# Kernel optimization log

Hardware: AMD Instinct MI355X
Metric: run time of the kernel (lower is better)

The kernel has to match this reference:

```python
import jax, jax.numpy as jnp
import numpy as np

N, D, L = 4096, 256, 3
E = 1.0  # eye scale 'e'


def _adj(X, W, b):
    # AdjLearner_intra: two Linear+ELU layers, then dense similarity h @ h.T -> [N, N]
    h = jax.nn.elu(X @ W[0] + b[0])
    h = jax.nn.elu(h @ W[1] + b[1])
    return h @ h.T


def _mlp(x, W, b, bn):
    # GIN MLP: Linear -> BatchNorm1d (batch stats, training mode) -> ReLU -> Linear
    h = x @ W[0] + b[0]
    mu = h.mean(axis=0)
    var = h.var(axis=0)  # biased, matches torch BN training normalization
    h = (h - mu) * jax.lax.rsqrt(var + 1e-5) * bn[0] + bn[1]
    return jax.nn.relu(h) @ W[1] + b[1]


def _gin(X, aW, ab, mW, mb, mbn):
    I = jnp.eye(X.shape[0], dtype=X.dtype)
    acc = jnp.zeros_like(X)
    for i in range(L):  # fixed small layer count
        adj = _adj(X, aW, ab)
        oh = (adj > adj.mean()).astype(X.dtype)  # adj_onehot: threshold at global mean
        X = _mlp((oh + E * I) @ X, mW[i], mb[i], mbn[i])
        acc = acc + X
    return acc / L


def setup_inputs() -> dict:
    key = jax.random.key(0)
    ks = jax.random.split(key, 16)
    s = np.float32(1.0 / np.sqrt(D))
    d = {}
    for i, name in enumerate(["QV", "Q", "V", "A"]):
        d[name] = jax.random.normal(ks[i], (N, D), jnp.float32)
    for j, br in enumerate(["qv", "t", "v"]):
        k0, k1 = ks[4 + 2 * j], ks[5 + 2 * j]
        d[f"adjW_{br}"] = jax.random.normal(k0, (2, D, D), jnp.float32) * s
        d[f"adjb_{br}"] = jnp.zeros((2, D), jnp.float32)
        d[f"mlpW_{br}"] = jax.random.normal(k1, (L, 2, D, D), jnp.float32) * s
        d[f"mlpb_{br}"] = jnp.zeros((L, 2, D), jnp.float32)
        d[f"mlpbn_{br}"] = jnp.stack(
            [jnp.ones((L, D), jnp.float32), jnp.zeros((L, D), jnp.float32)], axis=1
        )  # [L, 2(gamma,beta), D]
    return d


def reference(QV, Q, V, A,
              adjW_qv, adjb_qv, mlpW_qv, mlpb_qv, mlpbn_qv,
              adjW_t, adjb_t, mlpW_t, mlpb_t, mlpbn_t,
              adjW_v, adjb_v, mlpW_v, mlpb_v, mlpbn_v):
    GQV = _gin(QV, adjW_qv, adjb_qv, mlpW_qv, mlpb_qv, mlpbn_qv)  # type=1
    GQ = _gin(Q, adjW_t, adjb_t, mlpW_t, mlpb_t, mlpbn_t)          # type=2
    GV = _gin(V, adjW_v, adjb_v, mlpW_v, mlpb_v, mlpbn_v)          # type=3
    GA = _gin(A, adjW_t, adjb_t, mlpW_t, mlpb_t, mlpbn_t)          # type=2 (shared with Q branch)
    mse = lambda a, b: jnp.mean((a - b) ** 2)
    return (mse(GQV, GA), mse(GQ, GA), mse(GV, GA))
```

## Files before the change

### kernel.cpp

```cpp
#include <hip/hip_runtime.h>
#include <hip/hip_bf16.h>
#include <stdint.h>

#define NN 4096
#define DD 256
#define NL 3
typedef unsigned int uint;
typedef unsigned short ushort_t;

typedef float f32x4 __attribute__((ext_vector_type(4)));
typedef short bf16x8 __attribute__((ext_vector_type(8)));

struct Ptrs4 { const float* p0; const float* p1; const float* p2; const float* p3; };
__device__ __forceinline__ const float* sel(const Ptrs4& p, int b) {
    return b == 0 ? p.p0 : b == 1 ? p.p1 : b == 2 ? p.p2 : p.p3;
}

__device__ __forceinline__ uint pkbf2(float a, float b) {
    __hip_bfloat162 t = __float22bfloat162_rn(float2{a, b});
    union { __hip_bfloat162 h; uint u; } c; c.h = t; return c.u;
}
__device__ __forceinline__ void split3_pk(float a, float b, uint& h, uint& m, uint& l) {
    h = pkbf2(a, b);
    float ha = __uint_as_float(h << 16), hb = __uint_as_float(h & 0xFFFF0000u);
    float ra = a - ha, rb = b - hb;
    m = pkbf2(ra, rb);
    float ma = __uint_as_float(m << 16), mb = __uint_as_float(m & 0xFFFF0000u);
    l = pkbf2(ra - ma, rb - mb);
}

typedef __attribute__((address_space(3))) uint lds_u32;
typedef __attribute__((address_space(1))) const uint glb_u32;
__device__ __forceinline__ void gload16(void* l, const void* g) {
    __builtin_amdgcn_global_load_lds((glb_u32*)g, (lds_u32*)l, 16, 0, 0);
}
__device__ __forceinline__ void gload4(void* l, const void* g) {
    __builtin_amdgcn_global_load_lds((glb_u32*)g, (lds_u32*)l, 4, 0, 0);
}

template<int MODE>
__global__ __launch_bounds__(256, 4)
void gemm_small(const float* __restrict__ Xin, Ptrs4 Wp, Ptrs4 bp,
                float* __restrict__ Out, float* __restrict__ cs, float* __restrict__ csq,
                ushort_t* __restrict__ Hso)
{
    const int b = blockIdx.z;
    const float* Wb = sel(Wp, b);
    const float* bb = sel(bp, b);
    const float* X = Xin + (size_t)b * NN * DD;
    float* O = Out + (size_t)b * NN * DD;
    ushort_t* HsO = Hso + (size_t)b * 3 * (size_t)DD * NN;
    const int row0 = blockIdx.y * 128, col0 = blockIdx.x * 64;
    const int tid = threadIdx.x;
    __shared__ float Asm[16][132];
    __shared__ float Bsm[16][68];
    const int tr = (tid >> 4) << 3, tc = (tid & 15) << 2;
    const int m = tid & 127, kk = (tid >> 7) << 3;
    float acc[8][4] = {};
    for (int k0 = 0; k0 < DD; k0 += 16) {
        {
            const float* s1 = X + (size_t)(row0 + m) * DD + k0 + kk;
            float4 v0 = *(const float4*)s1, v1 = *(const float4*)(s1 + 4);
            Asm[kk+0][m]=v0.x; Asm[kk+1][m]=v0.y; Asm[kk+2][m]=v0.z; Asm[kk+3][m]=v0.w;
            Asm[kk+4][m]=v1.x; Asm[kk+5][m]=v1.y; Asm[kk+6][m]=v1.z; Asm[kk+7][m]=v1.w;
        }
        {
            const int k = tid >> 4, n = (tid & 15) << 2;
            *(float4*)&Bsm[k][n] = *(const float4*)(Wb + (size_t)(k0 + k) * DD + col0 + n);
        }
        __syncthreads();
        #pragma unroll
        for (int k = 0; k < 16; ++k) {
            float a[8], bv[4];
            *(float4*)&a[0] = *(const float4*)&Asm[k][tr];
            *(float4*)&a[4] = *(const float4*)&Asm[k][tr + 4];
            *(float4*)&bv[0] = *(const float4*)&Bsm[k][tc];
            #pragma unroll
            for (int i = 0; i < 8; ++i)
                #pragma unroll
                for (int j = 0; j < 4; ++j)
                    acc[i][j] = fmaf(a[i], bv[j], acc[i][j]);
        }
        __syncthreads();
    }
    float bias4[4];
    *(float4*)bias4 = *(const float4*)(bb + col0 + tc);
    float s4[4] = {0.f,0.f,0.f,0.f}, q4[4] = {0.f,0.f,0.f,0.f};
    const int dph = col0 + tc;
    const size_t sb3 = (size_t)(dph >> 3) * (NN * 8) + (dph & 4);
    #pragma unroll
    for (int i = 0; i < 8; ++i) {
        float ov[4];
        #pragma unroll
        for (int j = 0; j < 4; ++j) {
            float v = acc[i][j] + bias4[j];
            if (MODE == 0 || MODE == 1 || MODE == 3) v = (v > 0.f) ? v : (expf(v) - 1.f);
            ov[j] = v;
            if (MODE == 1 || MODE == 3) s4[j] += v;
            if (MODE == 2) { s4[j] += v; q4[j] += v * v; }
        }
        if (MODE == 3) {
            uint2 vh, vm, vl;
            split3_pk(ov[0], ov[1], vh.x, vm.x, vl.x);
            split3_pk(ov[2], ov[3], vh.y, vm.y, vl.y);
            size_t off = sb3 + (size_t)(row0 + tr + i) * 8;
            *(uint2*)(HsO + off) = vh;
            *(uint2*)(HsO + (size_t)DD * NN + off) = vm;
            *(uint2*)(HsO + (size_t)2 * DD * NN + off) = vl;
        } else {
            float4 o; o.x = ov[0]; o.y = ov[1]; o.z = ov[2]; o.w = ov[3];
            *(float4*)(O + (size_t)(row0 + tr + i) * DD + col0 + tc) = o;
        }
    }
    if (MODE == 1 || MODE == 2 || MODE == 3) {
        __syncthreads();
        const int rg = tid >> 4;
        #pragma unroll
        for (int j = 0; j < 4; ++j) {
            Asm[rg][tc + j] = s4[j];
            if (MODE == 2) Bsm[rg][tc + j] = q4[j];
        }
        __syncthreads();
        if (tid < 64) {
            float s = 0.f, q = 0.f;
            #pragma unroll
            for (int r = 0; r < 16; ++r) { s += Asm[r][tid]; if (MODE == 2) q += Bsm[r][tid]; }
            atomicAdd(&cs[b * DD + col0 + tid], s);
            if (MODE == 2) atomicAdd(&csq[b * DD + col0 + tid], q);
        }
    }
}

__global__ void thresh_k(const float* __restrict__ cs, float* __restrict__ tvals)
{
    const int b = blockIdx.x, t = threadIdx.x;
    __shared__ float red[256];
    float v = cs[b * DD + t];
    red[t] = v * v;
    __syncthreads();
    for (int s = 128; s > 0; s >>= 1) { if (t < s) red[t] += red[t + s]; __syncthreads(); }
    if (t == 0) tvals[b] = red[0] * (1.0f / 16777216.0f);
}

__global__ __launch_bounds__(256)
void tsplit_x(const float* __restrict__ Xin, ushort_t* __restrict__ Sh,
              ushort_t* __restrict__ Sm, ushort_t* __restrict__ Sl)
{
    const int b = blockIdx.z;
    const int n0 = blockIdx.x * 64, d0 = blockIdx.y * 64;
    const float* X = Xin + (size_t)b * NN * DD;
    __shared__ float ls[64][65];
    const int tid = threadIdx.x;
    #pragma unroll
    for (int i = 0; i < 4; ++i) {
        int u = (i << 8) + tid;
        int r = u >> 4, c4 = (u & 15) << 2;
        float4 v = *(const float4*)(X + (size_t)(n0 + r) * DD + d0 + c4);
        ls[r][c4] = v.x; ls[r][c4+1] = v.y; ls[r][c4+2] = v.z; ls[r][c4+3] = v.w;
    }
    __syncthreads();
    const int d = tid >> 2, seg = (tid & 3) << 4;
    uint ph[8], pm[8], pl[8];
    #pragma unroll
    for (int jj = 0; jj < 8; ++jj) {
        float a = ls[seg + 2 * jj][d];
        float c = ls[seg + 2 * jj + 1][d];
        split3_pk(a, c, ph[jj], pm[jj], pl[jj]);
    }
    size_t idx = ((size_t)(b * DD + d0 + d)) * NN + n0 + seg;
    *(uint4*)(Sh + idx)     = *(uint4*)&ph[0];
    *(uint4*)(Sh + idx + 8) = *(uint4*)&ph[4];
    *(uint4*)(Sm + idx)     = *(uint4*)&pm[0];
    *(uint4*)(Sm + idx + 8) = *(uint4*)&pm[4];
    *(uint4*)(Sl + idx)     = *(uint4*)&pl[0];
    *(uint4*)(Sl + idx + 8) = *(uint4*)&pl[4];
}

__global__ __launch_bounds__(256, 3)
void adj_mfma_s(const float* __restrict__ H, const float* __restrict__ tvals,
                uint8_t* __restrict__ mask)
{
    int t = blockIdx.x;
    int by = 0, rem = 32;
    while (t >= rem) { t -= rem; rem--; by++; }
    const int bx = by + t;
    const int b = blockIdx.z;
    const int row0 = by * 128, col0 = bx * 128;
    const int tid = threadIdx.x;
    const int wave = tid >> 6, ln = tid & 15, quad = (tid >> 4) & 3;
    const int wrow = wave >> 1, wcol = wave & 1;
    const float* Hb = H + (size_t)b * NN * DD;
    uint8_t* Mb = mask + (size_t)b * NN * (NN / 8);
    __shared__ ushort_t hs[2][3][128][34];

    f32x4 acc[4][4] = {};
    for (int k0 = 0; k0 < DD; k0 += 32) {
        #pragma unroll
        for (int i = 0; i < 8; ++i) {
            int f = (i << 8) + tid;
            int sr = f >> 3;
            int side = sr >> 7, r = sr & 127, part = f & 7;
            int grow = (side ? col0 : row0) + r;
            float4 v = *(const float4*)(Hb + (size_t)grow * DD + k0 + part * 4);
            uint h0, m0, l0, h1, m1, l1;
            split3_pk(v.x, v.y, h0, m0, l0);
            split3_pk(v.z, v.w, h1, m1, l1);
            uint2 ph; ph.x = h0; ph.y = h1;
            uint2 pm; pm.x = m0; pm.y = m1;
            uint2 pl; pl.x = l0; pl.y = l1;
            *(uint2*)&hs[side][0][r][part * 4] = ph;
            *(uint2*)&hs[side][1][r][part * 4] = pm;
            *(uint2*)&hs[side][2][r][part * 4] = pl;
        }
        __syncthreads();
        bf16x8 af[4][3];
        #pragma unroll
        for (int mt = 0; mt < 4; ++mt)
            #pragma unroll
            for (int lvl = 0; lvl < 3; ++lvl)
                af[mt][lvl] = *(const bf16x8*)&hs[0][lvl][wrow * 64 + mt * 16 + ln][quad * 8];
        #pragma unroll
        for (int nt = 0; nt < 4; ++nt) {
            int n = wcol * 64 + nt * 16 + ln;
            bf16x8 bh = *(const bf16x8*)&hs[1][0][n][quad * 8];
            bf16x8 bm = *(const bf16x8*)&hs[1][1][n][quad * 8];
            bf16x8 bl = *(const bf16x8*)&hs[1][2][n][quad * 8];
            #pragma unroll
            for (int mt = 0; mt < 4; ++mt) {
                f32x4 a = acc[mt][nt];
                a = __builtin_amdgcn_mfma_f32_16x16x32_bf16(af[mt][0], bh, a, 0, 0, 0);
                a = __builtin_amdgcn_mfma_f32_16x16x32_bf16(af[mt][0], bm, a, 0, 0, 0);
                a = __builtin_amdgcn_mfma_f32_16x16x32_bf16(af[mt][1], bh, a, 0, 0, 0);
                a = __builtin_amdgcn_mfma_f32_16x16x32_bf16(af[mt][0], bl, a, 0, 0, 0);
                a = __builtin_amdgcn_mfma_f32_16x16x32_bf16(af[mt][2], bh, a, 0, 0, 0);
                a = __builtin_amdgcn_mfma_f32_16x16x32_bf16(af[mt][1], bm, a, 0, 0, 0);
                acc[mt][nt] = a;
            }
        }
        __syncthreads();
    }
    const float t2 = tvals[b];
    #pragma unroll
    for (int mt = 0; mt < 4; ++mt)
        #pragma unroll
        for (int nt = 0; nt < 4; ++nt) {
            bool p0 = acc[mt][nt][0] > t2, p1 = acc[mt][nt][1] > t2;
            bool p2 = acc[mt][nt][2] > t2, p3 = acc[mt][nt][3] > t2;
            unsigned long long bal[4];
            bal[0] = __ballot(p0); bal[1] = __ballot(p1);
            bal[2] = __ballot(p2); bal[3] = __ballot(p3);
            if ((tid & 63) < 16) {
                int q = ln >> 2, rsel = ln & 3;
                unsigned long long bv = rsel == 0 ? bal[0] : rsel == 1 ? bal[1]
                                       : rsel == 2 ? bal[2] : bal[3];
                ushort_t u16 = (ushort_t)((bv >> (q * 16)) & 0xFFFFull);
                int row = row0 + wrow * 64 + mt * 16 + ln;
                int colb = (col0 + wcol * 64 + nt * 16) >> 3;
                *(ushort_t*)(Mb + (size_t)row * (NN / 8) + colb) = u16;
            }
            uint nib = (p0 ? 1u : 0u) | (p1 ? 2u : 0u) | (p2 ? 4u : 0u) | (p3 ? 8u : 0u);
            uint other = (uint)__shfl_xor((int)nib, 16);
            if ((quad & 1) == 0) {
                uint byt = nib | (other << 4);
                int rowm = col0 + wcol * 64 + nt * 16 + ln;
                int colbm = ((row0 + wrow * 64 + mt * 16) >> 3) + (quad >> 1);
                Mb[(size_t)rowm * (NN / 8) + colbm] = (uint8_t)byt;
            }
        }
}

__global__ __launch_bounds__(256, 3)
void adj_mfma_v2(const ushort_t* __restrict__ Hs, const float* __restrict__ tvals,
                 uint8_t* __restrict__ mask)
{
    int t = blockIdx.x;
    int by = 0, rem = 32;
    while (t >= rem) { t -= rem; rem--; by++; }
    const int bx = by + t;
    const int b = blockIdx.z;
    const int row0 = by * 128, col0 = bx * 128;
    const int tid = threadIdx.x;
    const int wave = tid >> 6, ln = tid & 15, quad = (tid >> 4) & 3;
    const int wrow = wave >> 1, wcol = wave & 1;
    const ushort_t* Hb = Hs + (size_t)b * 3 * (size_t)DD * NN;
    uint8_t* Mb = mask + (size_t)b * NN * (NN / 8);
    __shared__ ushort_t hs2[6][4][128][8];

    const int grow = tid & 127;
    const int qb = tid >> 7;
    const size_t var0 = (size_t)qb * (NN * 8) + (size_t)(row0 + grow) * 8;
    const size_t var1 = (size_t)qb * (NN * 8) + (size_t)(col0 + grow) * 8;

    f32x4 acc[4][4] = {};
    for (int kb0 = 0; kb0 < DD / 8; kb0 += 4) {
        #pragma unroll
        for (int c = 0; c < 12; ++c) {
            const int sl = c >> 1, part = c & 1;
            const int side = sl / 3, lvl = sl % 3;
            const ushort_t* g = Hb + (size_t)lvl * DD * NN
                                   + (size_t)(kb0 + part * 2) * (NN * 8)
                                   + (side ? var1 : var0);
            char* l = (char*)&hs2[0][0][0][0] + (((sl * 8 + part * 4 + wave)) << 10);
            gload16(l, g);
        }
        __syncthreads();
        bf16x8 af[4][3];
        #pragma unroll
        for (int mt = 0; mt < 4; ++mt)
            #pragma unroll
            for (int lvl = 0; lvl < 3; ++lvl)
                af[mt][lvl] = *(const bf16x8*)&hs2[lvl][quad][wrow * 64 + mt * 16 + ln][0];
        #pragma unroll
        for (int nt = 0; nt < 4; ++nt) {
            const int n = wcol * 64 + nt * 16 + ln;
            bf16x8 bh = *(const bf16x8*)&hs2[3][quad][n][0];
            bf16x8 bm = *(const bf16x8*)&hs2[4][quad][n][0];
            bf16x8 bl = *(const bf16x8*)&hs2[5][quad][n][0];
            #pragma unroll
            for (int mt = 0; mt < 4; ++mt) {
                f32x4 a = acc[mt][nt];
                a = __builtin_amdgcn_mfma_f32_16x16x32_bf16(af[mt][0], bh, a, 0, 0, 0);
                a = __builtin_amdgcn_mfma_f32_16x16x32_bf16(af[mt][0], bm, a, 0, 0, 0);
                a = __builtin_amdgcn_mfma_f32_16x16x32_bf16(af[mt][1], bh, a, 0, 0, 0);
                a = __builtin_amdgcn_mfma_f32_16x16x32_bf16(af[mt][0], bl, a, 0, 0, 0);
                a = __builtin_amdgcn_mfma_f32_16x16x32_bf16(af[mt][2], bh, a, 0, 0, 0);
                a = __builtin_amdgcn_mfma_f32_16x16x32_bf16(af[mt][1], bm, a, 0, 0, 0);
                acc[mt][nt] = a;
            }
        }
        __syncthreads();
    }
    const float t2 = tvals[b];
    #pragma unroll
    for (int mt = 0; mt < 4; ++mt)
        #pragma unroll
        for (int nt = 0; nt < 4; ++nt) {
            bool p0 = acc[mt][nt][0] > t2, p1 = acc[mt][nt][1] > t2;
            bool p2 = acc[mt][nt][2] > t2, p3 = acc[mt][nt][3] > t2;
            unsigned long long bal[4];
            bal[0] = __ballot(p0); bal[1] = __ballot(p1);
            bal[2] = __ballot(p2); bal[3] = __ballot(p3);
            if ((tid & 63) < 16) {
                int q = ln >> 2, rsel = ln & 3;
                unsigned long long bv = rsel == 0 ? bal[0] : rsel == 1 ? bal[1]
                                       : rsel == 2 ? bal[2] : bal[3];
                ushort_t u16 = (ushort_t)((bv >> (q * 16)) & 0xFFFFull);
                int row = row0 + wrow * 64 + mt * 16 + ln;
                int colb = (col0 + wcol * 64 + nt * 16) >> 3;
                *(ushort_t*)(Mb + (size_t)row * (NN / 8) + colb) = u16;
            }
            uint nib = (p0 ? 1u : 0u) | (p1 ? 2u : 0u) | (p2 ? 4u : 0u) | (p3 ? 8u : 0u);
            uint other = (uint)__shfl_xor((int)nib, 16);
            if ((quad & 1) == 0) {
                uint byt = nib | (other << 4);
                int rowm = col0 + wcol * 64 + nt * 16 + ln;
                int colbm = ((row0 + wrow * 64 + mt * 16) >> 3) + (quad >> 1);
                Mb[(size_t)rowm * (NN / 8) + colbm] = (uint8_t)byt;
            }
        }
}

__global__ __launch_bounds__(256)
void masked_mfma(float* __restrict__ Xio, const ushort_t* __restrict__ Sh,
                 const ushort_t* __restrict__ Sm, const ushort_t* __restrict__ Sl,
                 const uint8_t* __restrict__ mask)
{
    const int b = blockIdx.z;
    const int row0 = blockIdx.y * 128, col0 = blockIdx.x * 64;
    const int tid = threadIdx.x;
    const int wave = tid >> 6, ln = tid & 15, quad = (tid >> 4) & 3;
    const int wrow = wave >> 1, wcol = wave & 1;
    float* X = Xio + (size_t)b * NN * DD;
    const size_t sb = (size_t)b * DD * NN;
    const ushort_t* Ss[3] = { Sh + sb, Sm + sb, Sl + sb };
    const uint* Mw = (const uint*)(mask + (size_t)b * NN * (NN / 8));
    __shared__ ushort_t bt2[2][3][2][64][32];
    __shared__ uint msk2[2][2][128];

    const int c = tid >> 2;
    const int qp = (tid & 3) ^ ((tid >> 3) & 3);
    const size_t goff = (size_t)(col0 + c) * NN + (size_t)qp * 8;
    const size_t mrow = (size_t)(row0 + (tid & 127)) * 128;

    f32x4 acc[4][2] = {};

    #define STAGE(buf, t)                                                         \
        {                                                                         \
            const size_t j_ = (size_t)(t) * 64;                                   \
            _Pragma("unroll")                                                     \
            for (int lvl = 0; lvl < 3; ++lvl) {                                   \
                gload16((char*)&bt2[buf][lvl][0][0][0] + (wave << 10),            \
                        Ss[lvl] + goff + j_);                                     \
                gload16((char*)&bt2[buf][lvl][1][0][0] + (wave << 10),            \
                        Ss[lvl] + goff + j_ + 32);                                \
            }                                                                     \
            if (tid < 128) {                                                      \
                gload4((char*)&msk2[buf][0][0] + (wave << 8), Mw + mrow + 2*(t)); \
                gload4((char*)&msk2[buf][1][0] + (wave << 8), Mw + mrow + 2*(t)+1);\
            }                                                                     \
        }

    STAGE(0, 0);
    __syncthreads();

    for (int t = 0; t < NN / 64; ++t) {
        const int cur = t & 1;
        if (t < NN / 64 - 1) STAGE(cur ^ 1, t + 1);
        #pragma unroll
        for (int kk = 0; kk < 2; ++kk) {
            bf16x8 afr[4];
            #pragma unroll
            for (int mt = 0; mt < 4; ++mt) {
                uint w = msk2[cur][kk][wrow * 64 + mt * 16 + ln];
                uint byte = (w >> (quad * 8)) & 0xFFu;
                union { uint u[4]; bf16x8 v; } cv;
                #pragma unroll
                for (int p = 0; p < 4; ++p)
                    cv.u[p] = (((byte >> (2 * p)) & 1u) ? 0x3F80u : 0u) |
                              (((byte >> (2 * p + 1)) & 1u) ? 0x3F800000u : 0u);
                afr[mt] = cv.v;
            }
            #pragma unroll
            for (int nt = 0; nt < 2; ++nt) {
                const int n = wcol * 32 + nt * 16 + ln;
                const int slot = (quad ^ ((n >> 1) & 3)) * 8;
                bf16x8 bh = *(const bf16x8*)&bt2[cur][0][kk][n][slot];
                bf16x8 bm = *(const bf16x8*)&bt2[cur][1][kk][n][slot];
                bf16x8 bl = *(const bf16x8*)&bt2[cur][2][kk][n][slot];
                #pragma unroll
                for (int mt = 0; mt < 4; ++mt) {
                    f32x4 a = acc[mt][nt];
                    a = __builtin_amdgcn_mfma_f32_16x16x32_bf16(afr[mt], bh, a, 0, 0, 0);
                    a = __builtin_amdgcn_mfma_f32_16x16x32_bf16(afr[mt], bm, a, 0, 0, 0);
                    a = __builtin_amdgcn_mfma_f32_16x16x32_bf16(afr[mt], bl, a, 0, 0, 0);
                    acc[mt][nt] = a;
                }
            }
        }
        __syncthreads();
    }
    #undef STAGE
    #pragma unroll
    for (int mt = 0; mt < 4; ++mt)
        #pragma unroll
        for (int nt = 0; nt < 2; ++nt)
            #pragma unroll
            for (int r = 0; r < 4; ++r) {
                int row = row0 + wrow * 64 + mt * 16 + quad * 4 + r;
                int col = col0 + wcol * 32 + nt * 16 + ln;
                size_t idx = (size_t)row * DD + col;
                X[idx] = X[idx] + acc[mt][nt][r];
            }
}

__global__ __launch_bounds__(256, 4)
void gemm_bnrelu(const float* __restrict__ G, Ptrs4 Wp, Ptrs4 bp, Ptrs4 gbp,
                 const float* __restrict__ bns, const float* __restrict__ bnq,
                 float* __restrict__ Xout, float* __restrict__ accb, int first)
{
    const int b = blockIdx.z;
    const float* Wb = sel(Wp, b);
    const float* bb = sel(bp, b);
    const float* gb = sel(gbp, b);
    const float* Gb = G + (size_t)b * NN * DD;
    float* O = Xout + (size_t)b * NN * DD;
    float* Ab = accb + (size_t)b * NN * DD;
    const int row0 = blockIdx.y * 128, col0 = blockIdx.x * 64;
    const int tid = threadIdx.x;
    __shared__ float Asm[16][132];
    __shared__ float Bsm[16][68];
    __shared__ float scs[DD], shs[DD];
    {
        float mu = bns[b * DD + tid] * (1.0f / NN);
        float ms = bnq[b * DD + tid] * (1.0f / NN);
        float var = ms - mu * mu;
        float sc = gb[tid] / sqrtf(var + 1e-5f);
        scs[tid] = sc;
        shs[tid] = gb[DD + tid] - mu * sc;
    }
    __syncthreads();
    const int tr = (tid >> 4) << 3, tc = (tid & 15) << 2;
    const int m = tid & 127, kk = (tid >> 7) << 3;
    float acc[8][4] = {};
    for (int k0 = 0; k0 < DD; k0 += 16) {
        {
            const float* s1 = Gb + (size_t)(row0 + m) * DD + k0 + kk;
            float4 v0 = *(const float4*)s1, v1 = *(const float4*)(s1 + 4);
            float vv[8] = {v0.x, v0.y, v0.z, v0.w, v1.x, v1.y, v1.z, v1.w};
            #pragma unroll
            for (int i = 0; i < 8; ++i) {
                float v = fmaf(vv[i], scs[k0 + kk + i], shs[k0 + kk + i]);
                Asm[kk + i][m] = v > 0.f ? v : 0.f;
            }
        }
        {
            const int k = tid >> 4, n = (tid & 15) << 2;
            *(float4*)&Bsm[k][n] = *(const float4*)(Wb + (size_t)(k0 + k) * DD + col0 + n);
        }
        __syncthreads();
        #pragma unroll
        for (int k = 0; k < 16; ++k) {
            float a[8], bv[4];
            *(float4*)&a[0] = *(const float4*)&Asm[k][tr];
            *(float4*)&a[4] = *(const float4*)&Asm[k][tr + 4];
            *(float4*)&bv[0] = *(const float4*)&Bsm[k][tc];
            #pragma unroll
            for (int i = 0; i < 8; ++i)
                #pragma unroll
                for (int j = 0; j < 4; ++j)
                    acc[i][j] = fmaf(a[i], bv[j], acc[i][j]);
        }
        __syncthreads();
    }
    float bias4[4];
    *(float4*)bias4 = *(const float4*)(bb + col0 + tc);
    #pragma unroll
    for (int i = 0; i < 8; ++i) {
        size_t idx = (size_t)(row0 + tr + i) * DD + col0 + tc;
        float4 o;
        o.x = acc[i][0] + bias4[0]; o.y = acc[i][1] + bias4[1];
        o.z = acc[i][2] + bias4[2]; o.w = acc[i][3] + bias4[3];
        *(float4*)(O + idx) = o;
        if (first) {
            *(float4*)(Ab + idx) = o;
        } else {
            float4 p = *(const float4*)(Ab + idx);
            p.x += o.x; p.y += o.y; p.z += o.z; p.w += o.w;
            *(float4*)(Ab + idx) = p;
        }
    }
}

__global__ __launch_bounds__(256)
void mse_partial(const float* __restrict__ accb, double* __restrict__ msep)
{
    const int pair = blockIdx.x;
    const float* A_ = accb + (size_t)pair * NN * DD;
    const float* B_ = accb + (size_t)3 * NN * DD;
    const size_t total = (size_t)NN * DD;
    double s = 0.0;
    for (size_t i = (size_t)blockIdx.y * blockDim.x + threadIdx.x; i < total;
         i += (size_t)gridDim.y * blockDim.x) {
        float d = A_[i] - B_[i];
        s += (double)d * (double)d;
    }
    __shared__ double red[256];
    red[threadIdx.x] = s;
    __syncthreads();
    for (int st = 128; st > 0; st >>= 1) {
        if (threadIdx.x < st) red[threadIdx.x] += red[threadIdx.x + st];
        __syncthreads();
    }
    if (threadIdx.x == 0) atomicAdd(&msep[pair], red[0]);
}

__global__ void mse_final(const double* __restrict__ msep, float* __restrict__ out)
{
    int i = threadIdx.x;
    if (i < 3) out[i] = (float)(msep[i] / ((double)NN * DD) / 9.0);
}

static inline Ptrs4 mk4(const float* a, const float* b, const float* c, const float* d) {
    Ptrs4 p; p.p0 = a; p.p1 = b; p.p2 = c; p.p3 = d; return p;
}

extern "C" void kernel_launch(void* const* d_in, const int* in_sizes, int n_in,
                              void* d_out, int out_size, void* d_ws, size_t ws_size,
                              hipStream_t stream)
{
    (void)in_sizes; (void)n_in; (void)out_size;
    const float* adjW[3]  = {(const float*)d_in[4],  (const float*)d_in[9],  (const float*)d_in[14]};
    const float* adjb[3]  = {(const float*)d_in[5],  (const float*)d_in[10], (const float*)d_in[15]};
    const float* mlpW[3]  = {(const float*)d_in[6],  (const float*)d_in[11], (const float*)d_in[16]};
    const float* mlpb[3]  = {(const float*)d_in[7],  (const float*)d_in[12], (const float*)d_in[17]};
    const float* mlpbn[3] = {(const float*)d_in[8],  (const float*)d_in[13], (const float*)d_in[18]};

    char* ws = (char*)d_ws;
    double* msep  = (double*)ws;
    float* colsum = (float*)(ws + 64);
    float* bnsum  = colsum + 3 * 4 * DD;
    float* bnsq   = bnsum  + 3 * 4 * DD;
    float* tvals  = bnsq   + 3 * 4 * DD;
    const size_t tensN = (size_t)4 * NN * DD;
    const size_t HS_BYTES = (size_t)4 * 3 * DD * NN * 2;
    const size_t MASK_BYTES = (size_t)4 * NN * (NN / 8);

    float* Xbuf = (float*)(ws + 65536);
    float* Abuf = Xbuf + tensN;

    const size_t need_fast = 65536 + 2 * tensN * 4 + HS_BYTES + tensN * 4 + MASK_BYTES;
    const bool fast = ws_size >= need_fast;

    float* Bbuf = nullptr; float* accb; uint8_t* mask;
    ushort_t *Sh, *Sm, *Sl, *HsG = nullptr;
    if (fast) {
        char* hr = (char*)(Abuf + tensN);
        HsG  = (ushort_t*)hr;
        Sl   = (ushort_t*)hr;
        accb = (float*)(hr + HS_BYTES);
        mask = (uint8_t*)(accb + tensN);
    } else {
        Bbuf = Abuf + tensN;
        accb = Bbuf + tensN;
        mask = (uint8_t*)(accb + tensN);
        Sl   = (ushort_t*)Bbuf;
    }
    Sh = (ushort_t*)Abuf;
    Sm = Sh + tensN;

    hipMemsetAsync(ws, 0, 64 + 3 * 3 * 4 * DD * sizeof(float), stream);
    for (int b = 0; b < 4; ++b)
        hipMemcpyAsync(Xbuf + (size_t)b * NN * DD, d_in[b], (size_t)NN * DD * sizeof(float),
                       hipMemcpyDeviceToDevice, stream);

    dim3 gS(4, 32, 4);
    dim3 gA(528, 1, 4);
    dim3 gT(64, 4, 4);
    dim3 blk(256);

    for (int l = 0; l < NL; ++l) {
        float* cs_l = colsum + l * 4 * DD;
        float* bs_l = bnsum + l * 4 * DD;
        float* bq_l = bnsq  + l * 4 * DD;
        #define MK(arr, off) mk4(arr[0] + (off), arr[1] + (off), arr[2] + (off), arr[1] + (off))
        gemm_small<0><<<gS, blk, 0, stream>>>(Xbuf, MK(adjW, 0), MK(adjb, 0), Abuf,
                                              nullptr, nullptr, (ushort_t*)nullptr);
        if (fast) {
            gemm_small<3><<<gS, blk, 0, stream>>>(Abuf, MK(adjW, (size_t)DD * DD), MK(adjb, DD),
                                                  nullptr, cs_l, nullptr, HsG);
            thresh_k<<<4, blk, 0, stream>>>(cs_l, tvals);
            adj_mfma_v2<<<gA, blk, 0, stream>>>(HsG, tvals, mask);
        } else {
            gemm_small<1><<<gS, blk, 0, stream>>>(Abuf, MK(adjW, (size_t)DD * DD), MK(adjb, DD),
                                                  Bbuf, cs_l, nullptr, (ushort_t*)nullptr);
            thresh_k<<<4, blk, 0, stream>>>(cs_l, tvals);
            adj_mfma_s<<<gA, blk, 0, stream>>>(Bbuf, tvals, mask);
        }
        tsplit_x<<<gT, blk, 0, stream>>>(Xbuf, Sh, Sm, Sl);
        masked_mfma<<<gS, blk, 0, stream>>>(Xbuf, Sh, Sm, Sl, mask);
        const size_t w0 = (size_t)l * 2 * DD * DD, b0 = (size_t)l * 2 * DD;
        gemm_small<2><<<gS, blk, 0, stream>>>(Xbuf, MK(mlpW, w0), MK(mlpb, b0), Abuf,
                                              bs_l, bq_l, (ushort_t*)nullptr);
        gemm_bnrelu<<<gS, blk, 0, stream>>>(Abuf, MK(mlpW, w0 + (size_t)DD * DD), MK(mlpb, b0 + DD),
                                            MK(mlpbn, b0), bs_l, bq_l, Xbuf, accb, (l == 0) ? 1 : 0);
        #undef MK
    }
    mse_partial<<<dim3(3, 64), blk, 0, stream>>>(accb, msep);
    mse_final<<<1, 64, 0, stream>>>(msep, (float*)d_out);
}
```

Before: 1.208 ms.

## Double-buffer small GEMMs with async global-to-LDS loads and K=32 tiles

Both small fp32 GEMM kernels (gemm_small and gemm_bnrelu) now use two LDS buffers filled with global_load_lds direct copies, so the next K tile loads while the current one is computed. The A tile is kept row-major, and gemm_bnrelu moves its BN+ReLU into the inner loop, applied on read from LDS. Launch bounds drop from 4 to 2 blocks per SM to fit the larger shared memory. The row-major A layout turns each A fetch into 8 scalar LDS reads with a stride of 32 floats, which may cause bank conflicts. The BN transform is also recomputed by each thread that reads the same element.

```diff
diff --git a/kernel.cpp b/kernel.cpp
--- a/kernel.cpp
+++ b/kernel.cpp
@@ -39,7 +39,7 @@
 }
 
 template<int MODE>
-__global__ __launch_bounds__(256, 4)
+__global__ __launch_bounds__(256, 2)
 void gemm_small(const float* __restrict__ Xin, Ptrs4 Wp, Ptrs4 bp,
                 float* __restrict__ Out, float* __restrict__ cs, float* __restrict__ csq,
                 ushort_t* __restrict__ Hso)
@@ -52,29 +52,39 @@
     ushort_t* HsO = Hso + (size_t)b * 3 * (size_t)DD * NN;
     const int row0 = blockIdx.y * 128, col0 = blockIdx.x * 64;
     const int tid = threadIdx.x;
-    __shared__ float Asm[16][132];
-    __shared__ float Bsm[16][68];
+    const int wave = tid >> 6;
+    __shared__ float As[2][128][32];
+    __shared__ float Bs[2][32][64];
     const int tr = (tid >> 4) << 3, tc = (tid & 15) << 2;
-    const int m = tid & 127, kk = (tid >> 7) << 3;
+
+    #define GSTAGE(buf, k0_)                                                      \
+    {                                                                             \
+        _Pragma("unroll")                                                         \
+        for (int i = 0; i < 4; ++i) {                                             \
+            const int c = i * 256 + tid;                                          \
+            gload16((char*)&As[buf][0][0] + (size_t)(i * 256 + wave * 64) * 16,   \
+                    X + (size_t)(row0 + (c >> 3)) * DD + (k0_) + (c & 7) * 4);    \
+        }                                                                         \
+        _Pragma("unroll")                                                         \
+        for (int i = 0; i < 2; ++i) {                                             \
+            const int c = i * 256 + tid;                                          \
+            gload16((char*)&Bs[buf][0][0] + (size_t)(i * 256 + wave * 64) * 16,   \
+                    Wb + (size_t)((k0_) + (c >> 4)) * DD + col0 + (c & 15) * 4);  \
+        }                                                                         \
+    }
+
     float acc[8][4] = {};
-    for (int k0 = 0; k0 < DD; k0 += 16) {
-        {
-            const float* s1 = X + (size_t)(row0 + m) * DD + k0 + kk;
-            float4 v0 = *(const float4*)s1, v1 = *(const float4*)(s1 + 4);
-            Asm[kk+0][m]=v0.x; Asm[kk+1][m]=v0.y; Asm[kk+2][m]=v0.z; Asm[kk+3][m]=v0.w;
-            Asm[kk+4][m]=v1.x; Asm[kk+5][m]=v1.y; Asm[kk+6][m]=v1.z; Asm[kk+7][m]=v1.w;
-        }
-        {
-            const int k = tid >> 4, n = (tid & 15) << 2;
-            *(float4*)&Bsm[k][n] = *(const float4*)(Wb + (size_t)(k0 + k) * DD + col0 + n);
-        }
-        __syncthreads();
-        #pragma unroll
-        for (int k = 0; k < 16; ++k) {
+    GSTAGE(0, 0)
+    __syncthreads();
+    for (int t = 0; t < DD / 32; ++t) {
+        const int cur = t & 1;
+        if (t < DD / 32 - 1) GSTAGE(cur ^ 1, (t + 1) * 32)
+        #pragma unroll 8
+        for (int k = 0; k < 32; ++k) {
             float a[8], bv[4];
-            *(float4*)&a[0] = *(const float4*)&Asm[k][tr];
-            *(float4*)&a[4] = *(const float4*)&Asm[k][tr + 4];
-            *(float4*)&bv[0] = *(const float4*)&Bsm[k][tc];
+            *(float4*)&bv[0] = *(const float4*)&Bs[cur][k][tc];
+            #pragma unroll
+            for (int i = 0; i < 8; ++i) a[i] = As[cur][tr + i][k];
             #pragma unroll
             for (int i = 0; i < 8; ++i)
                 #pragma unroll
@@ -83,6 +93,8 @@
         }
         __syncthreads();
     }
+    #undef GSTAGE
+
     float bias4[4];
     *(float4*)bias4 = *(const float4*)(bb + col0 + tc);
     float s4[4] = {0.f,0.f,0.f,0.f}, q4[4] = {0.f,0.f,0.f,0.f};
@@ -113,18 +125,20 @@
         }
     }
     if (MODE == 1 || MODE == 2 || MODE == 3) {
+        float* scrS = &As[0][0][0];
+        float* scrQ = &Bs[0][0][0];
         __syncthreads();
         const int rg = tid >> 4;
         #pragma unroll
         for (int j = 0; j < 4; ++j) {
-            Asm[rg][tc + j] = s4[j];
-            if (MODE == 2) Bsm[rg][tc + j] = q4[j];
+            scrS[rg * 68 + tc + j] = s4[j];
+            if (MODE == 2) scrQ[rg * 68 + tc + j] = q4[j];
         }
         __syncthreads();
         if (tid < 64) {
             float s = 0.f, q = 0.f;
             #pragma unroll
-            for (int r = 0; r < 16; ++r) { s += Asm[r][tid]; if (MODE == 2) q += Bsm[r][tid]; }
+            for (int r = 0; r < 16; ++r) { s += scrS[r * 68 + tid]; if (MODE == 2) q += scrQ[r * 68 + tid]; }
             atomicAdd(&cs[b * DD + col0 + tid], s);
             if (MODE == 2) atomicAdd(&csq[b * DD + col0 + tid], q);
         }
@@ -453,7 +467,7 @@
             }
 }
 
-__global__ __launch_bounds__(256, 4)
+__global__ __launch_bounds__(256, 2)
 void gemm_bnrelu(const float* __restrict__ G, Ptrs4 Wp, Ptrs4 bp, Ptrs4 gbp,
                  const float* __restrict__ bns, const float* __restrict__ bnq,
                  float* __restrict__ Xout, float* __restrict__ accb, int first)
@@ -467,8 +481,9 @@
     float* Ab = accb + (size_t)b * NN * DD;
     const int row0 = blockIdx.y * 128, col0 = blockIdx.x * 64;
     const int tid = threadIdx.x;
-    __shared__ float Asm[16][132];
-    __shared__ float Bsm[16][68];
+    const int wave = tid >> 6;
+    __shared__ float As[2][128][32];
+    __shared__ float Bs[2][32][64];
     __shared__ float scs[DD], shs[DD];
     {
         float mu = bns[b * DD + tid] * (1.0f / NN);
@@ -478,32 +493,41 @@
         scs[tid] = sc;
         shs[tid] = gb[DD + tid] - mu * sc;
     }
+    const int tr = (tid >> 4) << 3, tc = (tid & 15) << 2;
+
+    #define GSTAGE(buf, k0_)                                                      \
+    {                                                                             \
+        _Pragma("unroll")                                                         \
+        for (int i = 0; i < 4; ++i) {                                             \
+            const int c = i * 256 + tid;                                          \
+            gload16((char*)&As[buf][0][0] + (size_t)(i * 256 + wave * 64) * 16,   \
+                    Gb + (size_t)(row0 + (c >> 3)) * DD + (k0_) + (c & 7) * 4);   \
+        }                                                                         \
+        _Pragma("unroll")                                                         \
+        for (int i = 0; i < 2; ++i) {                                             \
+            const int c = i * 256 + tid;                                          \
+            gload16((char*)&Bs[buf][0][0] + (size_t)(i * 256 + wave * 64) * 16,   \
+                    Wb + (size_t)((k0_) + (c >> 4)) * DD + col0 + (c & 15) * 4);  \
+        }                                                                         \
+    }
+
+    float acc[8][4] = {};
+    GSTAGE(0, 0)
     __syncthreads();
-    const int tr = (tid >> 4) << 3, tc = (tid & 15) << 2;
-    const int m = tid & 127, kk = (tid >> 7) << 3;
-    float acc[8][4] = {};
-    for (int k0 = 0; k0 < DD; k0 += 16) {
-        {
-            const float* s1 = Gb + (size_t)(row0 + m) * DD + k0 + kk;
-            float4 v0 = *(const float4*)s1, v1 = *(const float4*)(s1 + 4);
-            float vv[8] = {v0.x, v0.y, v0.z, v0.w, v1.x, v1.y, v1.z, v1.w};
+    for (int t = 0; t < DD / 32; ++t) {
+        const int cur = t & 1;
+        if (t < DD / 32 - 1) GSTAGE(cur ^ 1, (t + 1) * 32)
+        #pragma unroll 8
+        for (int k = 0; k < 32; ++k) {
+            const int kg = t * 32 + k;
+            const float sc = scs[kg], sh = shs[kg];
+            float a[8], bv[4];
+            *(float4*)&bv[0] = *(const float4*)&Bs[cur][k][tc];
             #pragma unroll
             for (int i = 0; i < 8; ++i) {
-                float v = fmaf(vv[i], scs[k0 + kk + i], shs[k0 + kk + i]);
-                Asm[kk + i][m] = v > 0.f ? v : 0.f;
-            }
-        }
-        {
-            const int k = tid >> 4, n = (tid & 15) << 2;
-            *(float4*)&Bsm[k][n] = *(const float4*)(Wb + (size_t)(k0 + k) * DD + col0 + n);
-        }
-        __syncthreads();
-        #pragma unroll
-        for (int k = 0; k < 16; ++k) {
-            float a[8], bv[4];
-            *(float4*)&a[0] = *(const float4*)&Asm[k][tr];
-            *(float4*)&a[4] = *(const float4*)&Asm[k][tr + 4];
-            *(float4*)&bv[0] = *(const float4*)&Bsm[k][tc];
+                float v = fmaf(As[cur][tr + i][k], sc, sh);
+                a[i] = v > 0.f ? v : 0.f;
+            }
             #pragma unroll
             for (int i = 0; i < 8; ++i)
                 #pragma unroll
@@ -512,6 +536,8 @@
         }
         __syncthreads();
     }
+    #undef GSTAGE
+
     float bias4[4];
     *(float4*)bias4 = *(const float4*)(bb + col0 + tc);
     #pragma unroll
```

After: 1.301 ms. +7.7%, slower.
